# Kernel optimization log

Measured on AMD Instinct MI355X. Metric: run time of the kernel, lower is better.

Reference implementation:

```python
import jax, jax.numpy as jnp
import numpy as np

B, D, NH = 32768, 32, 128
SCALE = 0.05  # weight init scale; keeps exp(s) well-conditioned


def setup_inputs() -> dict:
    key = jax.random.key(0)
    ks = jax.random.split(key, 10)
    x = jax.random.normal(ks[0], (B, D), jnp.float32)
    # layer 0: LeafParam(2) -> learned constant (s, t)
    p0 = jax.random.normal(ks[1], (2,), jnp.float32) * SCALE
    # per-dim MLPs for i = 1..D-1, stacked. Layer i consumes x[:, :i]; we pad
    # its first weight to (D, NH) with rows >= i zeroed so a single batched
    # einsum computes all per-dim nets at once (same math as the python loop).
    mask = (jnp.arange(D)[None, :] < jnp.arange(1, D)[:, None]).astype(jnp.float32)  # (D-1, D)
    W1 = jax.random.normal(ks[2], (D - 1, D, NH), jnp.float32) * SCALE * mask[:, :, None]
    b1 = jax.random.normal(ks[3], (D - 1, NH), jnp.float32) * SCALE
    W2 = jax.random.normal(ks[4], (D - 1, NH, NH), jnp.float32) * SCALE
    b2 = jax.random.normal(ks[5], (D - 1, NH), jnp.float32) * SCALE
    W3 = jax.random.normal(ks[6], (D - 1, NH, NH), jnp.float32) * SCALE
    b3 = jax.random.normal(ks[7], (D - 1, NH), jnp.float32) * SCALE
    W4 = jax.random.normal(ks[8], (D - 1, NH, 2), jnp.float32) * SCALE
    b4 = jax.random.normal(ks[9], (D - 1, 2), jnp.float32) * SCALE
    return dict(x=x, p0=p0, W1=W1, b1=b1, W2=W2, b2=b2, W3=W3, b3=b3, W4=W4, b4=b4)


def _lrelu(h):
    return jnp.where(h >= 0, h, 0.2 * h)  # LeakyReLU(0.2)


def reference(x, p0, W1, b1, W2, b2, W3, b3, W4, b4):
    # All D-1 per-dim MLPs in parallel. W1 rows >= i are zero, so
    h = _lrelu(jnp.einsum('bd,idh->bih', x, W1) + b1[None])     # (B, D-1, NH)
    h = _lrelu(jnp.einsum('bih,ihk->bik', h, W2) + b2[None])
    h = _lrelu(jnp.einsum('bih,ihk->bik', h, W3) + b3[None])
    st = jnp.einsum('bih,iho->bio', h, W4) + b4[None]           # (B, D-1, 2)
    st0 = jnp.broadcast_to(p0[None, None, :], (x.shape[0], 1, 2))
    st = jnp.concatenate([st0, st], axis=1)                     # (B, D, 2)
    s, t = st[..., 0], st[..., 1]
    z = x * jnp.exp(s) + t      # parity=True -> order is the identity permutation
    log_det = jnp.sum(s, axis=1)                                # (B,)
    return z, log_det
```

## Files before the change

kernel.cpp:

```cpp
#include <hip/hip_runtime.h>

typedef __bf16 v8bf  __attribute__((ext_vector_type(8)));
typedef float  f32x4  __attribute__((ext_vector_type(4)));
typedef float  f32x16 __attribute__((ext_vector_type(16)));
typedef unsigned int u32;
typedef u32 u32x4 __attribute__((ext_vector_type(4)));
typedef unsigned short u16;

#define NI   31
#define DD   32
#define NHID 128
#define NROW 32768
#define NCHUNK 64
#define ITERS  2
#define NET_EL 36864
#define W2F_EL 4096
#define W3F_EL 20480
#define LDS_W4T 73728
#define LDS_BB  74240
#define LDS_BYTES 74752

__device__ __forceinline__ u32 cvtpk(float lo, float hi) {
    u32 r;
    asm("v_cvt_pk_bf16_f32 %0, %1, %2" : "=v"(r) : "v"(lo), "v"(hi));
    return r;
}

__device__ __forceinline__ void repack_tile(const f32x16 c, v8bf* f0, v8bf* f1) {
    f32x16 v;
    #pragma unroll
    for (int r = 0; r < 16; ++r) { float x = c[r]; v[r] = fmaxf(x, 0.2f * x); }
    #pragma unroll
    for (int p = 0; p < 2; ++p) {
        u32 a0 = cvtpk(v[8*p + 0], v[8*p + 1]);
        u32 a1 = cvtpk(v[8*p + 2], v[8*p + 3]);
        u32 b0 = cvtpk(v[8*p + 4], v[8*p + 5]);
        u32 b1 = cvtpk(v[8*p + 6], v[8*p + 7]);
        asm("v_permlane32_swap_b32 %0, %1" : "+v"(a0), "+v"(b0));
        asm("v_permlane32_swap_b32 %0, %1" : "+v"(a1), "+v"(b1));
        u32x4 wd = {a0, a1, b0, b1};
        if (p == 0) *f0 = __builtin_bit_cast(v8bf, wd);
        else        *f1 = __builtin_bit_cast(v8bf, wd);
    }
}

__global__ void maf_prep(const float* __restrict__ W1, const float* __restrict__ W2,
                         const float* __restrict__ W3, const float* __restrict__ b1,
                         __bf16* __restrict__ blob,
                         __bf16* __restrict__ xfragB, __bf16* __restrict__ xfragA,
                         const float* __restrict__ x) {
    int b = blockIdx.x, t = threadIdx.x;
    if (b < 3 * NI) {
        __shared__ float panel[16 * 128];
        int kind = b / NI, i = b % NI;
        const float* src; __bf16* dst; int NKS;
        if (kind == 0)      { src = W2 + (size_t)i * NHID * NHID; dst = blob + (size_t)i * NET_EL + W2F_EL; NKS = 8; }
        else if (kind == 1) { src = W3 + (size_t)i * NHID * NHID; dst = blob + (size_t)i * NET_EL + W3F_EL; NKS = 8; }
        else                { src = W1 + (size_t)i * DD * NHID;   dst = blob + (size_t)i * NET_EL;          NKS = 2; }
        const int biasrow = (kind == 2) ? ((i <= 14) ? 15 : 31) : -1;
        const int fo = t & 127, hi2 = t >> 7;
        const int mt = fo >> 5, c = fo & 31;
        for (int ksb = 0; ksb < NKS; ++ksb) {
            #pragma unroll
            for (int r = 0; r < 8; ++r) {
                int e = r * 256 + t;
                int grow = ksb * 16 + (e >> 7), gcol = e & 127;
                float pv = src[(size_t)grow * NHID + gcol];
                if (grow == biasrow) pv = b1[i * NHID + gcol];
                panel[e] = pv;
            }
            __syncthreads();
            __bf16 tmp[8];
            #pragma unroll
            for (int j = 0; j < 8; ++j) tmp[j] = (__bf16)panel[(hi2 * 8 + j) * 128 + fo];
            *(u32x4*)&dst[((size_t)(mt * NKS + ksb) * 64 + hi2 * 32 + c) * 8] = *(u32x4*)tmp;
            __syncthreads();
        }
    } else {
        __shared__ float pan[64 * 33];
        const int xb = b - 3 * NI;
        for (int pass = 0; pass < 4; ++pass) {
            const int rb = xb * 256 + pass * 64;
            #pragma unroll
            for (int r = 0; r < 8; ++r) {
                int e = r * 256 + t;
                pan[(e >> 5) * 33 + (e & 31)] = x[(size_t)(rb + (e >> 5)) * DD + (e & 31)];
            }
            __syncthreads();
            {
                int w2 = t >> 6, l = t & 63;
                int nt = w2 >> 1, ks = w2 & 1;
                int c = l & 31, hi = l >> 5;
                float vb[8], va[8];
                #pragma unroll
                for (int j = 0; j < 8; ++j) {
                    int d = ks * 16 + hi * 8 + j;
                    float pv = pan[(nt * 32 + c) * 33 + d];
                    vb[j] = (d == 31) ? 1.0f : pv;
                    va[j] = (d == 15) ? 1.0f : pv;
                }
                u32x4 wb_ = {cvtpk(vb[0], vb[1]), cvtpk(vb[2], vb[3]),
                             cvtpk(vb[4], vb[5]), cvtpk(vb[6], vb[7])};
                *(u32x4*)&xfragB[(size_t)(rb >> 6) * 2048 + ((w2 * 64 + l) << 3)] = wb_;
                if (ks == 0) {
                    u32x4 wa_ = {cvtpk(va[0], va[1]), cvtpk(va[2], va[3]),
                                 cvtpk(va[4], va[5]), cvtpk(va[6], va[7])};
                    *(u32x4*)&xfragA[(size_t)(rb >> 6) * 1024 + ((nt * 64 + l) << 3)] = wa_;
                }
            }
            __syncthreads();
        }
    }
}

__global__ __launch_bounds__(256, 2) void maf_main(
    const __bf16* __restrict__ xfragB, const __bf16* __restrict__ xfragA,
    const __bf16* __restrict__ blob,
    const float* __restrict__ b2, const float* __restrict__ b3,
    const float* __restrict__ W4, const float* __restrict__ b4,
    float* __restrict__ sT, __bf16* __restrict__ tT) {

    extern __shared__ __align__(16) char smem[];
    __bf16* w4t = (__bf16*)(smem + LDS_W4T);
    __bf16* bb  = (__bf16*)(smem + LDS_BB);
    const __bf16* wlds = (const __bf16*)smem;

    const int t = threadIdx.x;
    const int i = blockIdx.x / NCHUNK;
    const int chunk = blockIdx.x % NCHUNK;
    const int l = t & 63, w = t >> 6, c = l & 31, hi = l >> 5;
    const bool use_k1 = (i >= 15);

    f32x16 acc[4][2];
    v8bf Bf[2][8];
    v8bf Bx[2][2];

#define LOADX(G)                                                                      \
    { if (use_k1) {                                                                   \
          const __bf16* xg = xfragB + (size_t)(G) * 2048;                             \
          Bx[0][0] = *(const v8bf*)&xg[(0 * 64 + l) << 3];                            \
          Bx[0][1] = *(const v8bf*)&xg[(1 * 64 + l) << 3];                            \
          Bx[1][0] = *(const v8bf*)&xg[(2 * 64 + l) << 3];                            \
          Bx[1][1] = *(const v8bf*)&xg[(3 * 64 + l) << 3];                            \
      } else {                                                                        \
          const __bf16* xg = xfragA + (size_t)(G) * 1024;                             \
          Bx[0][0] = *(const v8bf*)&xg[(0 * 64 + l) << 3];                            \
          Bx[1][0] = *(const v8bf*)&xg[(1 * 64 + l) << 3];                            \
      } }

    LOADX((chunk * (ITERS * 256) + w * 64) >> 6)

    {
        const u32x4* src = (const u32x4*)(blob + (size_t)i * NET_EL);
        u32x4* dst = (u32x4*)smem;
        #pragma unroll
        for (int k = 0; k < 18; ++k) dst[k * 256 + t] = src[k * 256 + t];
        w4t[t] = (__bf16)W4[(size_t)i * 2 * NHID + (t & 127) * 2 + (t >> 7)];
        if (t < NHID) {
            bb[t]       = (__bf16)b2[i * NHID + t];
            bb[128 + t] = (__bf16)b3[i * NHID + t];
        }
    }
    __syncthreads();

    const u32 ones0 = (hi == 0) ? 0x3F80u : 0u;
    const v8bf Bones = __builtin_bit_cast(v8bf, (u32x4){ones0, 0u, 0u, 0u});
    const float s0 = b4[2 * i], t0 = b4[2 * i + 1];
    const f32x16 zz = {};

    u32 Abw[2][4];
    #pragma unroll
    for (int L = 0; L < 2; ++L)
        #pragma unroll
        for (int mt = 0; mt < 4; ++mt)
            Abw[L][mt] = (hi == 0)
                ? (u32)__builtin_bit_cast(u16, bb[L * NHID + mt * 32 + c]) : 0u;

#define ABFRAG(L, MT) __builtin_bit_cast(v8bf, (u32x4){Abw[L][MT], 0u, 0u, 0u})

#define HIDDEN(BASE_EL, L)                                                            \
    {                                                                                 \
        _Pragma("unroll")                                                             \
        for (int mt = 0; mt < 4; ++mt)                                                \
            acc[mt][0] = __builtin_amdgcn_mfma_f32_32x32x16_bf16(                     \
                ABFRAG(L, mt), Bones, zz, 0, 0, 0);                                   \
        __builtin_amdgcn_s_setprio(1);                                                \
        _Pragma("unroll")                                                             \
        for (int ks = 0; ks < 8; ++ks) {                                              \
            v8bf A[4];                                                                \
            _Pragma("unroll")                                                         \
            for (int mt = 0; mt < 4; ++mt)                                            \
                A[mt] = *(const v8bf*)&wlds[(BASE_EL) + ((mt * 8 + ks) * 64 + l) * 8]; \
            if (ks == 0) {                                                            \
                _Pragma("unroll")                                                     \
                for (int mt = 0; mt < 4; ++mt) {                                      \
                    acc[mt][1] = __builtin_amdgcn_mfma_f32_32x32x16_bf16(             \
                        A[mt], Bf[1][0], acc[mt][0], 0, 0, 0);                        \
                    acc[mt][0] = __builtin_amdgcn_mfma_f32_32x32x16_bf16(             \
                        A[mt], Bf[0][0], acc[mt][0], 0, 0, 0);                        \
                }                                                                     \
            } else {                                                                  \
                _Pragma("unroll")                                                     \
                for (int mt = 0; mt < 4; ++mt)                                        \
                    _Pragma("unroll")                                                 \
                    for (int nt = 0; nt < 2; ++nt)                                    \
                        acc[mt][nt] = __builtin_amdgcn_mfma_f32_32x32x16_bf16(        \
                            A[mt], Bf[nt][ks], acc[mt][nt], 0, 0, 0);                 \
            }                                                                         \
        }                                                                             \
        __builtin_amdgcn_s_setprio(0);                                                \
        _Pragma("unroll")                                                             \
        for (int mt = 0; mt < 4; ++mt)                                                \
            _Pragma("unroll")                                                         \
            for (int nt = 0; nt < 2; ++nt)                                            \
                repack_tile(acc[mt][nt], &Bf[nt][2 * mt], &Bf[nt][2 * mt + 1]);       \
    }

    #pragma unroll 1
    for (int it = 0; it < ITERS; ++it) {
        const int row0 = chunk * (ITERS * 256) + it * 256 + w * 64;

        __builtin_amdgcn_s_setprio(1);
        #pragma unroll
        for (int mt = 0; mt < 4; ++mt) {
            v8bf A0 = *(const v8bf*)&wlds[((mt * 2 + 0) * 64 + l) * 8];
            v8bf A1;
            if (use_k1) A1 = *(const v8bf*)&wlds[((mt * 2 + 1) * 64 + l) * 8];
            #pragma unroll
            for (int nt = 0; nt < 2; ++nt) {
                f32x16 a = __builtin_amdgcn_mfma_f32_32x32x16_bf16(A0, Bx[nt][0], zz, 0, 0, 0);
                if (use_k1)
                    a = __builtin_amdgcn_mfma_f32_32x32x16_bf16(A1, Bx[nt][1], a, 0, 0, 0);
                acc[mt][nt] = a;
            }
        }
        __builtin_amdgcn_s_setprio(0);
        #pragma unroll
        for (int mt = 0; mt < 4; ++mt)
            #pragma unroll
            for (int nt = 0; nt < 2; ++nt)
                repack_tile(acc[mt][nt], &Bf[nt][2 * mt], &Bf[nt][2 * mt + 1]);

        if (it + 1 < ITERS)
            LOADX((chunk * (ITERS * 256) + (it + 1) * 256 + w * 64) >> 6)

        HIDDEN(W2F_EL, 0)
        HIDDEN(W3F_EL, 1)

        {
            f32x16 acc4[2];
            acc4[0] = zz; acc4[1] = zz;
            #pragma unroll
            for (int ks = 0; ks < 8; ++ks) {
                v8bf a4 = {};
                if (c < 2) a4 = *(const v8bf*)&w4t[c * NHID + ks * 16 + hi * 8];
                acc4[0] = __builtin_amdgcn_mfma_f32_32x32x16_bf16(a4, Bf[0][ks], acc4[0], 0, 0, 0);
                acc4[1] = __builtin_amdgcn_mfma_f32_32x32x16_bf16(a4, Bf[1][ks], acc4[1], 0, 0, 0);
            }
            if (hi == 0) {
                #pragma unroll
                for (int nt = 0; nt < 2; ++nt) {
                    int row = row0 + nt * 32 + c;
                    sT[(size_t)i * NROW + row] = acc4[nt][0] + s0;
                    tT[(size_t)i * NROW + row] = (__bf16)(acc4[nt][1] + t0);
                }
            }
        }
    }
#undef LOADX
#undef ABFRAG
#undef HIDDEN
}

__global__ void maf_fin(const float* __restrict__ x, const float* __restrict__ p0,
                        const float* __restrict__ sT, const __bf16* __restrict__ tT,
                        float* __restrict__ zout, float* __restrict__ ldout) {
    __shared__ float zsm[4 * 64 * 33];
    const int t = threadIdx.x, w = t >> 6, l = t & 63;
    const int rowbase = blockIdx.x * 256 + w * 64;
    const int row = rowbase + l;
    float* zs = zsm + w * (64 * 33);

    float xr[DD];
    #pragma unroll
    for (int q = 0; q < 8; ++q)
        *(f32x4*)&xr[q * 4] = *(const f32x4*)&x[(size_t)row * DD + q * 4];

    const float s0 = p0[0], t0 = p0[1];
    float ld = s0;
    zs[l * 33] = xr[0] * expf(s0) + t0;
    #pragma unroll
    for (int i = 0; i < NI; ++i) {
        float s  = sT[(size_t)i * NROW + row];
        float tt = (float)tT[(size_t)i * NROW + row];
        ld += s;
        zs[l * 33 + i + 1] = xr[i + 1] * expf(s) + tt;
    }
    ldout[row] = ld;
    #pragma unroll
    for (int j = 0; j < 32; ++j) {
        int f = j * 64 + l;
        zout[(size_t)rowbase * DD + f] = zs[(f >> 5) * 33 + (f & 31)];
    }
}

extern "C" void kernel_launch(void* const* d_in, const int* in_sizes, int n_in,
                              void* d_out, int out_size, void* d_ws, size_t ws_size,
                              hipStream_t stream) {
    (void)in_sizes; (void)n_in; (void)out_size; (void)ws_size;
    const float* x  = (const float*)d_in[0];
    const float* p0 = (const float*)d_in[1];
    const float* W1 = (const float*)d_in[2];
    const float* b1 = (const float*)d_in[3];
    const float* W2 = (const float*)d_in[4];
    const float* b2 = (const float*)d_in[5];
    const float* W3 = (const float*)d_in[6];
    const float* b3 = (const float*)d_in[7];
    const float* W4 = (const float*)d_in[8];
    const float* b4 = (const float*)d_in[9];

    float* zout  = (float*)d_out;
    float* ldout = zout + (size_t)NROW * DD;

    __bf16* blob   = (__bf16*)d_ws;
    __bf16* xfragB = blob + (size_t)NI * NET_EL;
    __bf16* xfragA = xfragB + (size_t)NROW * DD;
    float*  sT     = (float*)(xfragA + (size_t)NROW * 16);
    __bf16* tT     = (__bf16*)(sT + (size_t)NI * NROW);

    hipFuncSetAttribute((const void*)maf_main,
                        hipFuncAttributeMaxDynamicSharedMemorySize, LDS_BYTES);

    maf_prep<<<3 * NI + 128, 256, 0, stream>>>(W1, W2, W3, b1, blob, xfragB, xfragA, x);
    maf_main<<<NI * NCHUNK, 256, LDS_BYTES, stream>>>(xfragB, xfragA, blob,
                                                      b2, b3, W4, b4, sT, tT);
    maf_fin<<<NROW / 256, 256, 0, stream>>>(x, p0, sT, tT, zout, ldout);
}
```

Before: 102.6 us.

## Halve per-wave tile, stream W3 from global, shrink LDS for higher occupancy

Each wave now processes a single 32-row tile instead of two, which halves the accumulator and B-fragment register footprint. The grid doubles to 128 chunks per net. The W3 weights are no longer staged in LDS and are read straight from global memory with a double-buffered fragment prefetch, so static LDS drops to about 41 KB and launch bounds rise to 3 blocks per CU. In exchange each W2 fragment loaded from LDS is reused across half as many rows, and the W3 reads now depend on L2/global latency being hidden.

```diff
diff --git a/kernel.cpp b/kernel.cpp
--- a/kernel.cpp
+++ b/kernel.cpp
@@ -11,14 +11,11 @@
 #define DD   32
 #define NHID 128
 #define NROW 32768
-#define NCHUNK 64
+#define NCHUNK 128
 #define ITERS  2
 #define NET_EL 36864
 #define W2F_EL 4096
 #define W3F_EL 20480
-#define LDS_W4T 73728
-#define LDS_BB  74240
-#define LDS_BYTES 74752
 
 __device__ __forceinline__ u32 cvtpk(float lo, float hi) {
     u32 r;
@@ -113,48 +110,50 @@
     }
 }
 
-__global__ __launch_bounds__(256, 2) void maf_main(
+__global__ __launch_bounds__(256, 3) void maf_main(
     const __bf16* __restrict__ xfragB, const __bf16* __restrict__ xfragA,
     const __bf16* __restrict__ blob,
     const float* __restrict__ b2, const float* __restrict__ b3,
     const float* __restrict__ W4, const float* __restrict__ b4,
     float* __restrict__ sT, __bf16* __restrict__ tT) {
 
-    extern __shared__ __align__(16) char smem[];
-    __bf16* w4t = (__bf16*)(smem + LDS_W4T);
-    __bf16* bb  = (__bf16*)(smem + LDS_BB);
-    const __bf16* wlds = (const __bf16*)smem;
+    __shared__ __align__(16) __bf16 wlds[20480];
+    __shared__ __align__(16) __bf16 w4t[2 * NHID];
+    __shared__ __align__(16) __bf16 bb[2 * NHID];
 
     const int t = threadIdx.x;
-    const int i = blockIdx.x / NCHUNK;
-    const int chunk = blockIdx.x % NCHUNK;
+    const int i = blockIdx.x >> 7;
+    const int chunk = blockIdx.x & 127;
     const int l = t & 63, w = t >> 6, c = l & 31, hi = l >> 5;
     const bool use_k1 = (i >= 15);
-
-    f32x16 acc[4][2];
-    v8bf Bf[2][8];
-    v8bf Bx[2][2];
+    const int nt_sel = w & 1;
+
+    const __bf16* wg3 = blob + (size_t)i * NET_EL + W3F_EL;
+
+    f32x16 acc[4];
+    v8bf Bf[8];
+    v8bf Bx[2];
 
 #define LOADX(G)                                                                      \
     { if (use_k1) {                                                                   \
           const __bf16* xg = xfragB + (size_t)(G) * 2048;                             \
-          Bx[0][0] = *(const v8bf*)&xg[(0 * 64 + l) << 3];                            \
-          Bx[0][1] = *(const v8bf*)&xg[(1 * 64 + l) << 3];                            \
-          Bx[1][0] = *(const v8bf*)&xg[(2 * 64 + l) << 3];                            \
-          Bx[1][1] = *(const v8bf*)&xg[(3 * 64 + l) << 3];                            \
+          Bx[0] = *(const v8bf*)&xg[((nt_sel * 2 + 0) * 64 + l) << 3];                \
+          Bx[1] = *(const v8bf*)&xg[((nt_sel * 2 + 1) * 64 + l) << 3];                \
       } else {                                                                        \
           const __bf16* xg = xfragA + (size_t)(G) * 1024;                             \
-          Bx[0][0] = *(const v8bf*)&xg[(0 * 64 + l) << 3];                            \
-          Bx[1][0] = *(const v8bf*)&xg[(1 * 64 + l) << 3];                            \
+          Bx[0] = *(const v8bf*)&xg[(nt_sel * 64 + l) << 3];                          \
       } }
 
-    LOADX((chunk * (ITERS * 256) + w * 64) >> 6)
+    {
+        const int rb0 = chunk * 256 + w * 32;
+        LOADX(rb0 >> 6)
+    }
 
     {
         const u32x4* src = (const u32x4*)(blob + (size_t)i * NET_EL);
-        u32x4* dst = (u32x4*)smem;
-        #pragma unroll
-        for (int k = 0; k < 18; ++k) dst[k * 256 + t] = src[k * 256 + t];
+        u32x4* dst = (u32x4*)wlds;
+        #pragma unroll
+        for (int k = 0; k < 10; ++k) dst[k * 256 + t] = src[k * 256 + t];
         w4t[t] = (__bf16)W4[(size_t)i * 2 * NHID + (t & 127) * 2 + (t >> 7)];
         if (t < NHID) {
             bb[t]       = (__bf16)b2[i * NHID + t];
@@ -178,98 +177,96 @@
 
 #define ABFRAG(L, MT) __builtin_bit_cast(v8bf, (u32x4){Abw[L][MT], 0u, 0u, 0u})
 
-#define HIDDEN(BASE_EL, L)                                                            \
-    {                                                                                 \
-        _Pragma("unroll")                                                             \
-        for (int mt = 0; mt < 4; ++mt)                                                \
-            acc[mt][0] = __builtin_amdgcn_mfma_f32_32x32x16_bf16(                     \
-                ABFRAG(L, mt), Bones, zz, 0, 0, 0);                                   \
-        __builtin_amdgcn_s_setprio(1);                                                \
-        _Pragma("unroll")                                                             \
-        for (int ks = 0; ks < 8; ++ks) {                                              \
-            v8bf A[4];                                                                \
-            _Pragma("unroll")                                                         \
-            for (int mt = 0; mt < 4; ++mt)                                            \
-                A[mt] = *(const v8bf*)&wlds[(BASE_EL) + ((mt * 8 + ks) * 64 + l) * 8]; \
-            if (ks == 0) {                                                            \
-                _Pragma("unroll")                                                     \
-                for (int mt = 0; mt < 4; ++mt) {                                      \
-                    acc[mt][1] = __builtin_amdgcn_mfma_f32_32x32x16_bf16(             \
-                        A[mt], Bf[1][0], acc[mt][0], 0, 0, 0);                        \
-                    acc[mt][0] = __builtin_amdgcn_mfma_f32_32x32x16_bf16(             \
-                        A[mt], Bf[0][0], acc[mt][0], 0, 0, 0);                        \
-                }                                                                     \
-            } else {                                                                  \
-                _Pragma("unroll")                                                     \
-                for (int mt = 0; mt < 4; ++mt)                                        \
-                    _Pragma("unroll")                                                 \
-                    for (int nt = 0; nt < 2; ++nt)                                    \
-                        acc[mt][nt] = __builtin_amdgcn_mfma_f32_32x32x16_bf16(        \
-                            A[mt], Bf[nt][ks], acc[mt][nt], 0, 0, 0);                 \
-            }                                                                         \
-        }                                                                             \
-        __builtin_amdgcn_s_setprio(0);                                                \
-        _Pragma("unroll")                                                             \
-        for (int mt = 0; mt < 4; ++mt)                                                \
-            _Pragma("unroll")                                                         \
-            for (int nt = 0; nt < 2; ++nt)                                            \
-                repack_tile(acc[mt][nt], &Bf[nt][2 * mt], &Bf[nt][2 * mt + 1]);       \
-    }
-
     #pragma unroll 1
     for (int it = 0; it < ITERS; ++it) {
-        const int row0 = chunk * (ITERS * 256) + it * 256 + w * 64;
+        const int rowbase = chunk * 256 + it * 128 + w * 32;
 
         __builtin_amdgcn_s_setprio(1);
         #pragma unroll
         for (int mt = 0; mt < 4; ++mt) {
             v8bf A0 = *(const v8bf*)&wlds[((mt * 2 + 0) * 64 + l) * 8];
-            v8bf A1;
-            if (use_k1) A1 = *(const v8bf*)&wlds[((mt * 2 + 1) * 64 + l) * 8];
-            #pragma unroll
-            for (int nt = 0; nt < 2; ++nt) {
-                f32x16 a = __builtin_amdgcn_mfma_f32_32x32x16_bf16(A0, Bx[nt][0], zz, 0, 0, 0);
-                if (use_k1)
-                    a = __builtin_amdgcn_mfma_f32_32x32x16_bf16(A1, Bx[nt][1], a, 0, 0, 0);
-                acc[mt][nt] = a;
-            }
+            f32x16 a = __builtin_amdgcn_mfma_f32_32x32x16_bf16(A0, Bx[0], zz, 0, 0, 0);
+            if (use_k1) {
+                v8bf A1 = *(const v8bf*)&wlds[((mt * 2 + 1) * 64 + l) * 8];
+                a = __builtin_amdgcn_mfma_f32_32x32x16_bf16(A1, Bx[1], a, 0, 0, 0);
+            }
+            acc[mt] = a;
         }
         __builtin_amdgcn_s_setprio(0);
         #pragma unroll
         for (int mt = 0; mt < 4; ++mt)
-            #pragma unroll
-            for (int nt = 0; nt < 2; ++nt)
-                repack_tile(acc[mt][nt], &Bf[nt][2 * mt], &Bf[nt][2 * mt + 1]);
+            repack_tile(acc[mt], &Bf[2 * mt], &Bf[2 * mt + 1]);
 
         if (it + 1 < ITERS)
-            LOADX((chunk * (ITERS * 256) + (it + 1) * 256 + w * 64) >> 6)
-
-        HIDDEN(W2F_EL, 0)
-        HIDDEN(W3F_EL, 1)
+            LOADX((chunk * 256 + (it + 1) * 128 + w * 32) >> 6)
+
+        #pragma unroll
+        for (int mt = 0; mt < 4; ++mt)
+            acc[mt] = __builtin_amdgcn_mfma_f32_32x32x16_bf16(ABFRAG(0, mt), Bones, zz, 0, 0, 0);
+        __builtin_amdgcn_s_setprio(1);
+        #pragma unroll
+        for (int ks = 0; ks < 8; ++ks) {
+            v8bf A[4];
+            #pragma unroll
+            for (int mt = 0; mt < 4; ++mt)
+                A[mt] = *(const v8bf*)&wlds[W2F_EL + ((mt * 8 + ks) * 64 + l) * 8];
+            #pragma unroll
+            for (int mt = 0; mt < 4; ++mt)
+                acc[mt] = __builtin_amdgcn_mfma_f32_32x32x16_bf16(A[mt], Bf[ks], acc[mt], 0, 0, 0);
+        }
+        __builtin_amdgcn_s_setprio(0);
+        #pragma unroll
+        for (int mt = 0; mt < 4; ++mt)
+            repack_tile(acc[mt], &Bf[2 * mt], &Bf[2 * mt + 1]);
+
+#define LOADW3(DST, KS)                                                               \
+        { _Pragma("unroll")                                                           \
+          for (int mt = 0; mt < 4; ++mt)                                              \
+              DST[mt] = *(const v8bf*)&wg3[((mt * 8 + (KS)) * 64 + l) * 8]; }
+#define MFMA4(AF, BKS)                                                                \
+        { _Pragma("unroll")                                                           \
+          for (int mt = 0; mt < 4; ++mt)                                              \
+              acc[mt] = __builtin_amdgcn_mfma_f32_32x32x16_bf16(AF[mt], Bf[BKS], acc[mt], 0, 0, 0); }
 
         {
-            f32x16 acc4[2];
-            acc4[0] = zz; acc4[1] = zz;
+            v8bf Aa[4], Ab[4];
+            LOADW3(Aa, 0)
+            #pragma unroll
+            for (int mt = 0; mt < 4; ++mt)
+                acc[mt] = __builtin_amdgcn_mfma_f32_32x32x16_bf16(ABFRAG(1, mt), Bones, zz, 0, 0, 0);
+            __builtin_amdgcn_s_setprio(1);
+            #pragma unroll
+            for (int ks2 = 0; ks2 < 4; ++ks2) {
+                LOADW3(Ab, 2 * ks2 + 1)
+                MFMA4(Aa, 2 * ks2)
+                if (ks2 < 3) LOADW3(Aa, 2 * ks2 + 2)
+                MFMA4(Ab, 2 * ks2 + 1)
+            }
+            __builtin_amdgcn_s_setprio(0);
+        }
+        #pragma unroll
+        for (int mt = 0; mt < 4; ++mt)
+            repack_tile(acc[mt], &Bf[2 * mt], &Bf[2 * mt + 1]);
+
+        {
+            f32x16 acc4 = zz;
             #pragma unroll
             for (int ks = 0; ks < 8; ++ks) {
                 v8bf a4 = {};
                 if (c < 2) a4 = *(const v8bf*)&w4t[c * NHID + ks * 16 + hi * 8];
-                acc4[0] = __builtin_amdgcn_mfma_f32_32x32x16_bf16(a4, Bf[0][ks], acc4[0], 0, 0, 0);
-                acc4[1] = __builtin_amdgcn_mfma_f32_32x32x16_bf16(a4, Bf[1][ks], acc4[1], 0, 0, 0);
+                acc4 = __builtin_amdgcn_mfma_f32_32x32x16_bf16(a4, Bf[ks], acc4, 0, 0, 0);
             }
             if (hi == 0) {
-                #pragma unroll
-                for (int nt = 0; nt < 2; ++nt) {
-                    int row = row0 + nt * 32 + c;
-                    sT[(size_t)i * NROW + row] = acc4[nt][0] + s0;
-                    tT[(size_t)i * NROW + row] = (__bf16)(acc4[nt][1] + t0);
-                }
+                int row = rowbase + c;
+                sT[(size_t)i * NROW + row] = acc4[0] + s0;
+                tT[(size_t)i * NROW + row] = (__bf16)(acc4[1] + t0);
             }
         }
     }
 #undef LOADX
 #undef ABFRAG
-#undef HIDDEN
+#undef LOADW3
+#undef MFMA4
 }
 
 __global__ void maf_fin(const float* __restrict__ x, const float* __restrict__ p0,
@@ -328,11 +325,8 @@
     float*  sT     = (float*)(xfragA + (size_t)NROW * 16);
     __bf16* tT     = (__bf16*)(sT + (size_t)NI * NROW);
 
-    hipFuncSetAttribute((const void*)maf_main,
-                        hipFuncAttributeMaxDynamicSharedMemorySize, LDS_BYTES);
-
     maf_prep<<<3 * NI + 128, 256, 0, stream>>>(W1, W2, W3, b1, blob, xfragB, xfragA, x);
-    maf_main<<<NI * NCHUNK, 256, LDS_BYTES, stream>>>(xfragB, xfragA, blob,
-                                                      b2, b3, W4, b4, sT, tT);
+    maf_main<<<NI * NCHUNK, 256, 0, stream>>>(xfragB, xfragA, blob,
+                                              b2, b3, W4, b4, sT, tT);
     maf_fin<<<NROW / 256, 256, 0, stream>>>(x, p0, sT, tT, zout, ldout);
 }
```

Result: slower. 214.8 us (+109.3%).

## Split hidden layers per N-tile to interleave repack with MFMA work

Applied to the files above, without the earlier changes.

Each hidden layer and the output layer are now processed one 32-column N-tile at a time. The repack of one tile is placed before the MFMA chain of the same layer on the other tile, so VALU conversion work can overlap matrix-core execution instead of running as a serial phase. The first-K-step accumulator reuse trick is removed. The cost is that each weight A-fragment is now read from LDS twice, once per tile, and each MFMA chain only has 4 independent accumulators instead of 8, which may expose MFMA dependency latency.

```diff
diff --git a/kernel.cpp b/kernel.cpp
--- a/kernel.cpp
+++ b/kernel.cpp
@@ -178,11 +178,11 @@
 
 #define ABFRAG(L, MT) __builtin_bit_cast(v8bf, (u32x4){Abw[L][MT], 0u, 0u, 0u})
 
-#define HIDDEN(BASE_EL, L)                                                            \
+#define HIDDEN_S(BASE_EL, L, NT)                                                      \
     {                                                                                 \
         _Pragma("unroll")                                                             \
         for (int mt = 0; mt < 4; ++mt)                                                \
-            acc[mt][0] = __builtin_amdgcn_mfma_f32_32x32x16_bf16(                     \
+            acc[mt][NT] = __builtin_amdgcn_mfma_f32_32x32x16_bf16(                    \
                 ABFRAG(L, mt), Bones, zz, 0, 0, 0);                                   \
         __builtin_amdgcn_s_setprio(1);                                                \
         _Pragma("unroll")                                                             \
@@ -191,29 +191,33 @@
             _Pragma("unroll")                                                         \
             for (int mt = 0; mt < 4; ++mt)                                            \
                 A[mt] = *(const v8bf*)&wlds[(BASE_EL) + ((mt * 8 + ks) * 64 + l) * 8]; \
-            if (ks == 0) {                                                            \
-                _Pragma("unroll")                                                     \
-                for (int mt = 0; mt < 4; ++mt) {                                      \
-                    acc[mt][1] = __builtin_amdgcn_mfma_f32_32x32x16_bf16(             \
-                        A[mt], Bf[1][0], acc[mt][0], 0, 0, 0);                        \
-                    acc[mt][0] = __builtin_amdgcn_mfma_f32_32x32x16_bf16(             \
-                        A[mt], Bf[0][0], acc[mt][0], 0, 0, 0);                        \
-                }                                                                     \
-            } else {                                                                  \
-                _Pragma("unroll")                                                     \
-                for (int mt = 0; mt < 4; ++mt)                                        \
-                    _Pragma("unroll")                                                 \
-                    for (int nt = 0; nt < 2; ++nt)                                    \
-                        acc[mt][nt] = __builtin_amdgcn_mfma_f32_32x32x16_bf16(        \
-                            A[mt], Bf[nt][ks], acc[mt][nt], 0, 0, 0);                 \
-            }                                                                         \
+            _Pragma("unroll")                                                         \
+            for (int mt = 0; mt < 4; ++mt)                                            \
+                acc[mt][NT] = __builtin_amdgcn_mfma_f32_32x32x16_bf16(                \
+                    A[mt], Bf[NT][ks], acc[mt][NT], 0, 0, 0);                         \
         }                                                                             \
         __builtin_amdgcn_s_setprio(0);                                                \
+    }
+
+#define REPACK(NT)                                                                    \
+    { _Pragma("unroll")                                                               \
+      for (int mt = 0; mt < 4; ++mt)                                                  \
+          repack_tile(acc[mt][NT], &Bf[NT][2 * mt], &Bf[NT][2 * mt + 1]); }
+
+#define L4_S(NT, ROW0)                                                                \
+    {                                                                                 \
+        f32x16 acc4 = zz;                                                             \
         _Pragma("unroll")                                                             \
-        for (int mt = 0; mt < 4; ++mt)                                                \
-            _Pragma("unroll")                                                         \
-            for (int nt = 0; nt < 2; ++nt)                                            \
-                repack_tile(acc[mt][nt], &Bf[nt][2 * mt], &Bf[nt][2 * mt + 1]);       \
+        for (int ks = 0; ks < 8; ++ks) {                                              \
+            v8bf a4 = {};                                                             \
+            if (c < 2) a4 = *(const v8bf*)&w4t[c * NHID + ks * 16 + hi * 8];          \
+            acc4 = __builtin_amdgcn_mfma_f32_32x32x16_bf16(a4, Bf[NT][ks], acc4, 0, 0, 0); \
+        }                                                                             \
+        if (hi == 0) {                                                                \
+            int row = (ROW0) + (NT) * 32 + c;                                         \
+            sT[(size_t)i * NROW + row] = acc4[0] + s0;                                \
+            tT[(size_t)i * NROW + row] = (__bf16)(acc4[1] + t0);                      \
+        }                                                                             \
     }
 
     #pragma unroll 1
@@ -235,41 +239,28 @@
             }
         }
         __builtin_amdgcn_s_setprio(0);
-        #pragma unroll
-        for (int mt = 0; mt < 4; ++mt)
-            #pragma unroll
-            for (int nt = 0; nt < 2; ++nt)
-                repack_tile(acc[mt][nt], &Bf[nt][2 * mt], &Bf[nt][2 * mt + 1]);
 
         if (it + 1 < ITERS)
             LOADX((chunk * (ITERS * 256) + (it + 1) * 256 + w * 64) >> 6)
 
-        HIDDEN(W2F_EL, 0)
-        HIDDEN(W3F_EL, 1)
-
-        {
-            f32x16 acc4[2];
-            acc4[0] = zz; acc4[1] = zz;
-            #pragma unroll
-            for (int ks = 0; ks < 8; ++ks) {
-                v8bf a4 = {};
-                if (c < 2) a4 = *(const v8bf*)&w4t[c * NHID + ks * 16 + hi * 8];
-                acc4[0] = __builtin_amdgcn_mfma_f32_32x32x16_bf16(a4, Bf[0][ks], acc4[0], 0, 0, 0);
-                acc4[1] = __builtin_amdgcn_mfma_f32_32x32x16_bf16(a4, Bf[1][ks], acc4[1], 0, 0, 0);
-            }
-            if (hi == 0) {
-                #pragma unroll
-                for (int nt = 0; nt < 2; ++nt) {
-                    int row = row0 + nt * 32 + c;
-                    sT[(size_t)i * NROW + row] = acc4[nt][0] + s0;
-                    tT[(size_t)i * NROW + row] = (__bf16)(acc4[nt][1] + t0);
-                }
-            }
-        }
+        REPACK(0)
+        HIDDEN_S(W2F_EL, 0, 0)
+        REPACK(1)
+        HIDDEN_S(W2F_EL, 0, 1)
+        REPACK(0)
+        HIDDEN_S(W3F_EL, 1, 0)
+        REPACK(1)
+        HIDDEN_S(W3F_EL, 1, 1)
+        REPACK(0)
+        L4_S(0, row0)
+        REPACK(1)
+        L4_S(1, row0)
     }
 #undef LOADX
 #undef ABFRAG
-#undef HIDDEN
+#undef HIDDEN_S
+#undef REPACK
+#undef L4_S
 }
 
 __global__ void maf_fin(const float* __restrict__ x, const float* __restrict__ p0,
```

Result: slower. 114.8 us (+11.9%).

## Shrink per-wave tile to 32 rows, use 384-thread blocks for occupancy

Applied to the files above, without the earlier changes.

Each wave now handles one 32-row column tile per iteration instead of two, which halves the accumulator and B-fragment register footprint. Blocks grow to 6 waves with launch bounds of 3 blocks per CU, and the per-network grid changes from 64 to 86 chunks, with bounds checks for the ragged tail. The aim is more resident waves to hide MFMA and LDS latency, at the cost of reading each A weight fragment from LDS for half as many MFMAs. It also adds some idle waves in the last chunk.

```diff
diff --git a/kernel.cpp b/kernel.cpp
--- a/kernel.cpp
+++ b/kernel.cpp
@@ -11,8 +11,8 @@
 #define DD   32
 #define NHID 128
 #define NROW 32768
-#define NCHUNK 64
-#define ITERS  2
+#define NBLK 86
+#define ITERS 2
 #define NET_EL 36864
 #define W2F_EL 4096
 #define W3F_EL 20480
@@ -113,7 +113,7 @@
     }
 }
 
-__global__ __launch_bounds__(256, 2) void maf_main(
+__global__ __launch_bounds__(384, 3) void maf_main(
     const __bf16* __restrict__ xfragB, const __bf16* __restrict__ xfragA,
     const __bf16* __restrict__ blob,
     const float* __restrict__ b2, const float* __restrict__ b3,
@@ -126,36 +126,36 @@
     const __bf16* wlds = (const __bf16*)smem;
 
     const int t = threadIdx.x;
-    const int i = blockIdx.x / NCHUNK;
-    const int chunk = blockIdx.x % NCHUNK;
+    const int i = blockIdx.x / NBLK;
+    const int chunk = blockIdx.x % NBLK;
     const int l = t & 63, w = t >> 6, c = l & 31, hi = l >> 5;
     const bool use_k1 = (i >= 15);
-
-    f32x16 acc[4][2];
-    v8bf Bf[2][8];
-    v8bf Bx[2][2];
-
-#define LOADX(G)                                                                      \
-    { if (use_k1) {                                                                   \
-          const __bf16* xg = xfragB + (size_t)(G) * 2048;                             \
-          Bx[0][0] = *(const v8bf*)&xg[(0 * 64 + l) << 3];                            \
-          Bx[0][1] = *(const v8bf*)&xg[(1 * 64 + l) << 3];                            \
-          Bx[1][0] = *(const v8bf*)&xg[(2 * 64 + l) << 3];                            \
-          Bx[1][1] = *(const v8bf*)&xg[(3 * 64 + l) << 3];                            \
+    const int g0 = chunk * 12 + w * 2;
+
+    f32x16 acc[4];
+    v8bf Bf[8];
+    v8bf Bx[2];
+
+#define LOADX(GG)                                                                     \
+    { const int G_ = (GG) >> 1, nt_ = (GG) & 1;                                       \
+      if (use_k1) {                                                                   \
+          const __bf16* xg = xfragB + (size_t)G_ * 2048;                              \
+          Bx[0] = *(const v8bf*)&xg[((nt_ * 2 + 0) * 64 + l) << 3];                   \
+          Bx[1] = *(const v8bf*)&xg[((nt_ * 2 + 1) * 64 + l) << 3];                   \
       } else {                                                                        \
-          const __bf16* xg = xfragA + (size_t)(G) * 1024;                             \
-          Bx[0][0] = *(const v8bf*)&xg[(0 * 64 + l) << 3];                            \
-          Bx[1][0] = *(const v8bf*)&xg[(1 * 64 + l) << 3];                            \
+          const __bf16* xg = xfragA + (size_t)G_ * 1024;                              \
+          Bx[0] = *(const v8bf*)&xg[(nt_ * 64 + l) << 3];                             \
       } }
 
-    LOADX((chunk * (ITERS * 256) + w * 64) >> 6)
+    if (g0 < 1024) LOADX(g0)
 
     {
         const u32x4* src = (const u32x4*)(blob + (size_t)i * NET_EL);
         u32x4* dst = (u32x4*)smem;
         #pragma unroll
-        for (int k = 0; k < 18; ++k) dst[k * 256 + t] = src[k * 256 + t];
-        w4t[t] = (__bf16)W4[(size_t)i * 2 * NHID + (t & 127) * 2 + (t >> 7)];
+        for (int k = 0; k < 12; ++k) dst[k * 384 + t] = src[k * 384 + t];
+        if (t < 256)
+            w4t[t] = (__bf16)W4[(size_t)i * 2 * NHID + (t & 127) * 2 + (t >> 7)];
         if (t < NHID) {
             bb[t]       = (__bf16)b2[i * NHID + t];
             bb[128 + t] = (__bf16)b3[i * NHID + t];
@@ -182,7 +182,7 @@
     {                                                                                 \
         _Pragma("unroll")                                                             \
         for (int mt = 0; mt < 4; ++mt)                                                \
-            acc[mt][0] = __builtin_amdgcn_mfma_f32_32x32x16_bf16(                     \
+            acc[mt] = __builtin_amdgcn_mfma_f32_32x32x16_bf16(                        \
                 ABFRAG(L, mt), Bones, zz, 0, 0, 0);                                   \
         __builtin_amdgcn_s_setprio(1);                                                \
         _Pragma("unroll")                                                             \
@@ -191,79 +191,56 @@
             _Pragma("unroll")                                                         \
             for (int mt = 0; mt < 4; ++mt)                                            \
                 A[mt] = *(const v8bf*)&wlds[(BASE_EL) + ((mt * 8 + ks) * 64 + l) * 8]; \
-            if (ks == 0) {                                                            \
-                _Pragma("unroll")                                                     \
-                for (int mt = 0; mt < 4; ++mt) {                                      \
-                    acc[mt][1] = __builtin_amdgcn_mfma_f32_32x32x16_bf16(             \
-                        A[mt], Bf[1][0], acc[mt][0], 0, 0, 0);                        \
-                    acc[mt][0] = __builtin_amdgcn_mfma_f32_32x32x16_bf16(             \
-                        A[mt], Bf[0][0], acc[mt][0], 0, 0, 0);                        \
-                }                                                                     \
-            } else {                                                                  \
-                _Pragma("unroll")                                                     \
-                for (int mt = 0; mt < 4; ++mt)                                        \
-                    _Pragma("unroll")                                                 \
-                    for (int nt = 0; nt < 2; ++nt)                                    \
-                        acc[mt][nt] = __builtin_amdgcn_mfma_f32_32x32x16_bf16(        \
-                            A[mt], Bf[nt][ks], acc[mt][nt], 0, 0, 0);                 \
-            }                                                                         \
+            _Pragma("unroll")                                                         \
+            for (int mt = 0; mt < 4; ++mt)                                            \
+                acc[mt] = __builtin_amdgcn_mfma_f32_32x32x16_bf16(                    \
+                    A[mt], Bf[ks], acc[mt], 0, 0, 0);                                 \
         }                                                                             \
         __builtin_amdgcn_s_setprio(0);                                                \
         _Pragma("unroll")                                                             \
         for (int mt = 0; mt < 4; ++mt)                                                \
-            _Pragma("unroll")                                                         \
-            for (int nt = 0; nt < 2; ++nt)                                            \
-                repack_tile(acc[mt][nt], &Bf[nt][2 * mt], &Bf[nt][2 * mt + 1]);       \
+            repack_tile(acc[mt], &Bf[2 * mt], &Bf[2 * mt + 1]);                       \
     }
 
     #pragma unroll 1
     for (int it = 0; it < ITERS; ++it) {
-        const int row0 = chunk * (ITERS * 256) + it * 256 + w * 64;
+        const int g = g0 + it;
+        if (g >= 1024) continue;
 
         __builtin_amdgcn_s_setprio(1);
         #pragma unroll
         for (int mt = 0; mt < 4; ++mt) {
             v8bf A0 = *(const v8bf*)&wlds[((mt * 2 + 0) * 64 + l) * 8];
-            v8bf A1;
-            if (use_k1) A1 = *(const v8bf*)&wlds[((mt * 2 + 1) * 64 + l) * 8];
-            #pragma unroll
-            for (int nt = 0; nt < 2; ++nt) {
-                f32x16 a = __builtin_amdgcn_mfma_f32_32x32x16_bf16(A0, Bx[nt][0], zz, 0, 0, 0);
-                if (use_k1)
-                    a = __builtin_amdgcn_mfma_f32_32x32x16_bf16(A1, Bx[nt][1], a, 0, 0, 0);
-                acc[mt][nt] = a;
-            }
+            f32x16 a = __builtin_amdgcn_mfma_f32_32x32x16_bf16(A0, Bx[0], zz, 0, 0, 0);
+            if (use_k1) {
+                v8bf A1 = *(const v8bf*)&wlds[((mt * 2 + 1) * 64 + l) * 8];
+                a = __builtin_amdgcn_mfma_f32_32x32x16_bf16(A1, Bx[1], a, 0, 0, 0);
+            }
+            acc[mt] = a;
         }
         __builtin_amdgcn_s_setprio(0);
         #pragma unroll
         for (int mt = 0; mt < 4; ++mt)
-            #pragma unroll
-            for (int nt = 0; nt < 2; ++nt)
-                repack_tile(acc[mt][nt], &Bf[nt][2 * mt], &Bf[nt][2 * mt + 1]);
-
-        if (it + 1 < ITERS)
-            LOADX((chunk * (ITERS * 256) + (it + 1) * 256 + w * 64) >> 6)
+            repack_tile(acc[mt], &Bf[2 * mt], &Bf[2 * mt + 1]);
+
+        if (it + 1 < ITERS && g + 1 < 1024)
+            LOADX(g + 1)
 
         HIDDEN(W2F_EL, 0)
         HIDDEN(W3F_EL, 1)
 
         {
-            f32x16 acc4[2];
-            acc4[0] = zz; acc4[1] = zz;
+            f32x16 acc4 = zz;
             #pragma unroll
             for (int ks = 0; ks < 8; ++ks) {
                 v8bf a4 = {};
                 if (c < 2) a4 = *(const v8bf*)&w4t[c * NHID + ks * 16 + hi * 8];
-                acc4[0] = __builtin_amdgcn_mfma_f32_32x32x16_bf16(a4, Bf[0][ks], acc4[0], 0, 0, 0);
-                acc4[1] = __builtin_amdgcn_mfma_f32_32x32x16_bf16(a4, Bf[1][ks], acc4[1], 0, 0, 0);
+                acc4 = __builtin_amdgcn_mfma_f32_32x32x16_bf16(a4, Bf[ks], acc4, 0, 0, 0);
             }
             if (hi == 0) {
-                #pragma unroll
-                for (int nt = 0; nt < 2; ++nt) {
-                    int row = row0 + nt * 32 + c;
-                    sT[(size_t)i * NROW + row] = acc4[nt][0] + s0;
-                    tT[(size_t)i * NROW + row] = (__bf16)(acc4[nt][1] + t0);
-                }
+                int row = g * 32 + c;
+                sT[(size_t)i * NROW + row] = acc4[0] + s0;
+                tT[(size_t)i * NROW + row] = (__bf16)(acc4[1] + t0);
             }
         }
     }
@@ -332,7 +309,7 @@
                         hipFuncAttributeMaxDynamicSharedMemorySize, LDS_BYTES);
 
     maf_prep<<<3 * NI + 128, 256, 0, stream>>>(W1, W2, W3, b1, blob, xfragB, xfragA, x);
-    maf_main<<<NI * NCHUNK, 256, LDS_BYTES, stream>>>(xfragB, xfragA, blob,
-                                                      b2, b3, W4, b4, sT, tT);
+    maf_main<<<NI * NBLK, 384, LDS_BYTES, stream>>>(xfragB, xfragA, blob,
+                                                    b2, b3, W4, b4, sT, tT);
     maf_fin<<<NROW / 256, 256, 0, stream>>>(x, p0, sT, tT, zout, ldout);
 }
```

Measured after the change: 128.7 us. +25.4%, slower.
